# Kernel tuning notes

Measured on AMD Instinct MI355X. Metric: run time of the kernel, lower is better.

The kernel has to match this reference:

```python
import jax, jax.numpy as jnp
import numpy as np

B, TGT, SRC = 16, 1024, 1024
TGT_DIM, SRC_DIM = 1024, 1024


def setup_inputs() -> dict:
    key = jax.random.key(0)
    k1, k2, k3, k4 = jax.random.split(key, 4)
    source = jax.random.normal(k1, (B, TGT, TGT_DIM), dtype=jnp.float32)
    memory_bank = jax.random.normal(k2, (B, SRC, SRC_DIM), dtype=jnp.float32)
    # lengths in [1, SRC] so every row has at least one valid position
    memory_lengths = jax.random.randint(k3, (B,), 1, SRC + 1)
    # nn.Linear(tgt_enc_dim, src_enc_dim, bias=False): weight [src_dim, tgt_dim]
    W_in = jax.random.normal(k4, (SRC_DIM, TGT_DIM), dtype=jnp.float32) / np.sqrt(TGT_DIM)
    return {"source": source, "memory_bank": memory_bank,
            "memory_lengths": memory_lengths, "W_in": W_in}


def reference(source, memory_bank, memory_lengths, W_in):
    # general attention: score = (h_t W_in^T) @ h_s^T
    h_t = jnp.einsum('btd,ed->bte', source, W_in)          # [B, TGT, SRC_DIM]
    align = jnp.einsum('bte,bse->bts', h_t, memory_bank)   # [B, TGT, SRC]
    # sequence mask: valid where j < length
    valid = jnp.arange(SRC)[None, :] < memory_lengths[:, None]  # [B, SRC]
    align = jnp.where(valid[:, None, :], align, -jnp.inf)
    return jax.nn.softmax(align, axis=-1)                  # [B, TGT, SRC]
```

## Files before the change

kernel.cpp:

```cpp
#include <hip/hip_runtime.h>
#include <hip/hip_bf16.h>

typedef __bf16 bf16;
typedef __bf16 bf16x8 __attribute__((ext_vector_type(8)));
typedef __bf16 bf16x4 __attribute__((ext_vector_type(4)));
typedef float  f32x4  __attribute__((ext_vector_type(4)));
typedef float  f32x16 __attribute__((ext_vector_type(16)));

struct hl { bf16 h, l; };
__device__ __forceinline__ hl split1(float v) {
    hl r;
    r.h = (bf16)v;
    r.l = (bf16)(v - (float)r.h);
    return r;
}

__device__ __forceinline__ void glds16(const void* g, void* l) {
    __builtin_amdgcn_global_load_lds(
        (const __attribute__((address_space(1))) void*)g,
        (__attribute__((address_space(3))) void*)l, 16, 0, 0);
}

template<int AMODE, int BMODE, int OMODE>
__global__ __launch_bounds__(256, 4) void gemm3(
    const float* __restrict__ Af, const bf16* __restrict__ Agh, const bf16* __restrict__ Agl,
    const float* __restrict__ Bf, const bf16* __restrict__ Bgh, const bf16* __restrict__ Bgl,
    float* __restrict__ Cf, bf16* __restrict__ Cgh, bf16* __restrict__ Cgl,
    int M, int N, int K, long sAz, long sBz, long sCz, int nbm, int nbn)
{
    constexpr int LDA = AMODE ? 32 : 40;
    constexpr int LDB = BMODE ? 32 : 40;
    __shared__ __align__(16) bf16 Ah[128 * LDA];
    __shared__ __align__(16) bf16 Al[128 * LDA];
    __shared__ __align__(16) bf16 Bh[128 * LDB];
    __shared__ __align__(16) bf16 Bl[128 * LDB];

    const int tid  = threadIdx.x;
    const int lane = tid & 63;
    const int wid  = tid >> 6;
    const int wm   = wid >> 1;
    const int wn   = wid & 1;

    const int qq = gridDim.x >> 3;
    const int sw = (blockIdx.x & 7) * qq + (blockIdx.x >> 3);
    const int z  = sw / (nbm * nbn);
    const int tt = sw % (nbm * nbn);
    const int m0 = (tt / nbn) * 128;
    const int n0 = (tt % nbn) * 128;

    const int r0  = tid >> 2;
    const int c0s = ((((tid & 3) * 16) ^ ((r0 & 6) << 3)) >> 1);

    const float* aF[4]; const float* bF[4];
    const bf16 *aH0, *aH1, *aL0, *aL1, *bH0, *bH1, *bL0, *bL1;
    if constexpr (AMODE == 0) {
#pragma unroll
        for (int j = 0; j < 4; ++j) {
            const int idx = j * 256 + tid;
            aF[j] = Af + (long)z * sAz + (long)(m0 + (idx >> 3)) * K + (idx & 7) * 4;
        }
    } else {
        aH0 = Agh + (long)z * sAz + (long)(m0 + r0) * K + c0s;
        aH1 = aH0 + (long)64 * K;
        aL0 = Agl + (long)z * sAz + (long)(m0 + r0) * K + c0s;
        aL1 = aL0 + (long)64 * K;
    }
    if constexpr (BMODE == 0) {
#pragma unroll
        for (int j = 0; j < 4; ++j) {
            const int idx = j * 256 + tid;
            bF[j] = Bf + (long)z * sBz + (long)(n0 + (idx >> 3)) * K + (idx & 7) * 4;
        }
    } else {
        bH0 = Bgh + (long)z * sBz + (long)(n0 + r0) * K + c0s;
        bH1 = bH0 + (long)64 * K;
        bL0 = Bgl + (long)z * sBz + (long)(n0 + r0) * K + c0s;
        bL1 = bL0 + (long)64 * K;
    }

    const int lr32 = lane & 31;
    const int kb8  = (lane >> 5) * 8;
    const int swA  = AMODE ? ((lr32 & 6) << 2) : 0;
    const int swB  = BMODE ? ((lr32 & 6) << 2) : 0;
    const int aRow0 = (wm * 64 + lr32) * LDA;
    const int aRow1 = aRow0 + 32 * LDA;
    const int bRow0 = (wn * 64 + lr32) * LDB;
    const int bRow1 = bRow0 + 32 * LDB;

    f32x16 acc[2][2];
#pragma unroll
    for (int i = 0; i < 2; ++i)
#pragma unroll
        for (int j = 0; j < 2; ++j) acc[i][j] = (f32x16)0.0f;

    for (int kt = 0; kt < K; kt += 32) {
        __syncthreads();
        if constexpr (AMODE == 1) {
            glds16(aH0, &Ah[tid * 8]); glds16(aH1, &Ah[(256 + tid) * 8]);
            glds16(aL0, &Al[tid * 8]); glds16(aL1, &Al[(256 + tid) * 8]);
            aH0 += 32; aH1 += 32; aL0 += 32; aL1 += 32;
        } else {
#pragma unroll
            for (int j = 0; j < 4; ++j) {
                const int idx = j * 256 + tid;
                const int r = idx >> 3, c = (idx & 7) * 4;
                const float4 v = *(const float4*)aF[j]; aF[j] += 32;
                bf16x4 h, l;
                hl s0 = split1(v.x); h.x = s0.h; l.x = s0.l;
                hl s1 = split1(v.y); h.y = s1.h; l.y = s1.l;
                hl s2 = split1(v.z); h.z = s2.h; l.z = s2.l;
                hl s3 = split1(v.w); h.w = s3.h; l.w = s3.l;
                *(bf16x4*)&Ah[r * LDA + c] = h;
                *(bf16x4*)&Al[r * LDA + c] = l;
            }
        }
        if constexpr (BMODE == 1) {
            glds16(bH0, &Bh[tid * 8]); glds16(bH1, &Bh[(256 + tid) * 8]);
            glds16(bL0, &Bl[tid * 8]); glds16(bL1, &Bl[(256 + tid) * 8]);
            bH0 += 32; bH1 += 32; bL0 += 32; bL1 += 32;
        } else {
#pragma unroll
            for (int j = 0; j < 4; ++j) {
                const int idx = j * 256 + tid;
                const int r = idx >> 3, c = (idx & 7) * 4;
                const float4 v = *(const float4*)bF[j]; bF[j] += 32;
                bf16x4 h, l;
                hl s0 = split1(v.x); h.x = s0.h; l.x = s0.l;
                hl s1 = split1(v.y); h.y = s1.h; l.y = s1.l;
                hl s2 = split1(v.z); h.z = s2.h; l.z = s2.l;
                hl s3 = split1(v.w); h.w = s3.h; l.w = s3.l;
                *(bf16x4*)&Bh[r * LDB + c] = h;
                *(bf16x4*)&Bl[r * LDB + c] = l;
            }
        }
        __syncthreads();

#pragma unroll
        for (int kk = 0; kk < 2; ++kk) {
            const int ca = (kk * 16 + kb8) ^ swA;
            const int cb = (kk * 16 + kb8) ^ swB;
            bf16x8 ah0 = *(const bf16x8*)&Ah[aRow0 + ca];
            bf16x8 ah1 = *(const bf16x8*)&Ah[aRow1 + ca];
            bf16x8 al0 = *(const bf16x8*)&Al[aRow0 + ca];
            bf16x8 al1 = *(const bf16x8*)&Al[aRow1 + ca];
            bf16x8 bh0 = *(const bf16x8*)&Bh[bRow0 + cb];
            bf16x8 bh1 = *(const bf16x8*)&Bh[bRow1 + cb];
            bf16x8 bl0 = *(const bf16x8*)&Bl[bRow0 + cb];
            bf16x8 bl1 = *(const bf16x8*)&Bl[bRow1 + cb];

            acc[0][0] = __builtin_amdgcn_mfma_f32_32x32x16_bf16(ah0, bh0, acc[0][0], 0, 0, 0);
            acc[0][1] = __builtin_amdgcn_mfma_f32_32x32x16_bf16(ah0, bh1, acc[0][1], 0, 0, 0);
            acc[1][0] = __builtin_amdgcn_mfma_f32_32x32x16_bf16(ah1, bh0, acc[1][0], 0, 0, 0);
            acc[1][1] = __builtin_amdgcn_mfma_f32_32x32x16_bf16(ah1, bh1, acc[1][1], 0, 0, 0);

            acc[0][0] = __builtin_amdgcn_mfma_f32_32x32x16_bf16(al0, bh0, acc[0][0], 0, 0, 0);
            acc[0][1] = __builtin_amdgcn_mfma_f32_32x32x16_bf16(al0, bh1, acc[0][1], 0, 0, 0);
            acc[1][0] = __builtin_amdgcn_mfma_f32_32x32x16_bf16(al1, bh0, acc[1][0], 0, 0, 0);
            acc[1][1] = __builtin_amdgcn_mfma_f32_32x32x16_bf16(al1, bh1, acc[1][1], 0, 0, 0);

            acc[0][0] = __builtin_amdgcn_mfma_f32_32x32x16_bf16(ah0, bl0, acc[0][0], 0, 0, 0);
            acc[0][1] = __builtin_amdgcn_mfma_f32_32x32x16_bf16(ah0, bl1, acc[0][1], 0, 0, 0);
            acc[1][0] = __builtin_amdgcn_mfma_f32_32x32x16_bf16(ah1, bl0, acc[1][0], 0, 0, 0);
            acc[1][1] = __builtin_amdgcn_mfma_f32_32x32x16_bf16(ah1, bl1, acc[1][1], 0, 0, 0);
        }
    }

    const int drow = 4 * (lane >> 5);
#pragma unroll
    for (int i = 0; i < 2; ++i)
#pragma unroll
        for (int j = 0; j < 2; ++j) {
            f32x16 a = acc[i][j];
#pragma unroll
            for (int q = 0; q < 16; ++q) {
                const int row = m0 + wm * 64 + i * 32 + (q & 3) + 8 * (q >> 2) + drow;
                const int col = n0 + wn * 64 + j * 32 + lr32;
                const long off = (long)z * sCz + (long)row * N + col;
                if constexpr (OMODE == 0) {
                    Cf[off] = a[q];
                } else {
                    hl s = split1(a[q]);
                    Cgh[off] = s.h; Cgl[off] = s.l;
                }
            }
        }
}

__global__ __launch_bounds__(256) void split_pair(
    const float* __restrict__ x, bf16* __restrict__ h, bf16* __restrict__ l, long n4)
{
    long i = (long)blockIdx.x * 256 + threadIdx.x;
    const long stride = (long)gridDim.x * 256;
    for (; i < n4; i += stride) {
        const float4 v = ((const float4*)x)[i];
        bf16x4 hh, ll;
        hl s0 = split1(v.x); hh.x = s0.h; ll.x = s0.l;
        hl s1 = split1(v.y); hh.y = s1.h; ll.y = s1.l;
        hl s2 = split1(v.z); hh.z = s2.h; ll.z = s2.l;
        hl s3 = split1(v.w); hh.w = s3.h; ll.w = s3.l;
        ((bf16x4*)h)[i] = hh;
        ((bf16x4*)l)[i] = ll;
    }
}

__global__ __launch_bounds__(256) void softmax_wave(
    float* __restrict__ data, const int* __restrict__ lens)
{
    const int tid  = threadIdx.x;
    const int lane = tid & 63;
    const int row  = blockIdx.x * 4 + (tid >> 6);
    const int len  = lens[row >> 10];
    float* p = data + (long)row * 1024;

    float4 v[4];
#pragma unroll
    for (int q = 0; q < 4; ++q) v[q] = *(const float4*)(p + 4 * (lane + 64 * q));

    float m = -INFINITY;
#pragma unroll
    for (int q = 0; q < 4; ++q) {
        const int base = 4 * (lane + 64 * q);
        if (base + 0 < len) m = fmaxf(m, v[q].x);
        if (base + 1 < len) m = fmaxf(m, v[q].y);
        if (base + 2 < len) m = fmaxf(m, v[q].z);
        if (base + 3 < len) m = fmaxf(m, v[q].w);
    }
#pragma unroll
    for (int off = 32; off >= 1; off >>= 1) m = fmaxf(m, __shfl_xor(m, off));

    float s = 0.0f;
    float4 e[4];
#pragma unroll
    for (int q = 0; q < 4; ++q) {
        const int base = 4 * (lane + 64 * q);
        e[q].x = (base + 0 < len) ? __expf(v[q].x - m) : 0.0f;
        e[q].y = (base + 1 < len) ? __expf(v[q].y - m) : 0.0f;
        e[q].z = (base + 2 < len) ? __expf(v[q].z - m) : 0.0f;
        e[q].w = (base + 3 < len) ? __expf(v[q].w - m) : 0.0f;
        s += e[q].x + e[q].y + e[q].z + e[q].w;
    }
#pragma unroll
    for (int off = 32; off >= 1; off >>= 1) s += __shfl_xor(s, off);

    const float inv = 1.0f / s;
#pragma unroll
    for (int q = 0; q < 4; ++q) {
        float4 o; o.x = e[q].x * inv; o.y = e[q].y * inv; o.z = e[q].z * inv; o.w = e[q].w * inv;
        *(float4*)(p + 4 * (lane + 64 * q)) = o;
    }
}

__global__ __launch_bounds__(256) void gemm_bt_split(
    const float* __restrict__ A, const float* __restrict__ Bmat,
    float* __restrict__ C, int M, int N, int K,
    long sAz, long sBz, long sCz)
{
    __shared__ __align__(16) bf16 Ah[128][40];
    __shared__ __align__(16) bf16 Al[128][40];
    __shared__ __align__(16) bf16 Bh[128][40];
    __shared__ __align__(16) bf16 Bl[128][40];

    const int tid  = threadIdx.x;
    const int lane = tid & 63;
    const int wid  = tid >> 6;
    const int wm   = wid >> 1;
    const int wn   = wid & 1;
    const int z    = blockIdx.z;
    const long aBase = (long)z * sAz;
    const long bBase = (long)z * sBz;
    const long cBase = (long)z * sCz;
    const int m0 = blockIdx.x * 128;
    const int n0 = blockIdx.y * 128;

    f32x4 acc[4][4];
#pragma unroll
    for (int i = 0; i < 4; ++i)
#pragma unroll
        for (int j = 0; j < 4; ++j) acc[i][j] = (f32x4)0.0f;

    const int lr = lane & 15;
    const int lk = (lane >> 4) * 8;

    for (int kt = 0; kt < K; kt += 32) {
        __syncthreads();
#pragma unroll
        for (int j = 0; j < 4; ++j) {
            const int idx = j * 256 + tid;
            const int r   = idx >> 3;
            const int c   = (idx & 7) * 4;
            const float4 va = *(const float4*)(A    + aBase + (long)(m0 + r) * K + kt + c);
            const float4 vb = *(const float4*)(Bmat + bBase + (long)(n0 + r) * K + kt + c);
            bf16x4 ah, al, bh, bl;
            hl a0 = split1(va.x); ah.x = a0.h; al.x = a0.l;
            hl a1 = split1(va.y); ah.y = a1.h; al.y = a1.l;
            hl a2 = split1(va.z); ah.z = a2.h; al.z = a2.l;
            hl a3 = split1(va.w); ah.w = a3.h; al.w = a3.l;
            hl b0 = split1(vb.x); bh.x = b0.h; bl.x = b0.l;
            hl b1 = split1(vb.y); bh.y = b1.h; bl.y = b1.l;
            hl b2 = split1(vb.z); bh.z = b2.h; bl.z = b2.l;
            hl b3 = split1(vb.w); bh.w = b3.h; bl.w = b3.l;
            *(bf16x4*)&Ah[r][c] = ah; *(bf16x4*)&Al[r][c] = al;
            *(bf16x4*)&Bh[r][c] = bh; *(bf16x4*)&Bl[r][c] = bl;
        }
        __syncthreads();

        bf16x8 afh[4], afl[4], bfh[4], bfl[4];
#pragma unroll
        for (int i = 0; i < 4; ++i) {
            afh[i] = *(const bf16x8*)&Ah[wm * 64 + i * 16 + lr][lk];
            afl[i] = *(const bf16x8*)&Al[wm * 64 + i * 16 + lr][lk];
            bfh[i] = *(const bf16x8*)&Bh[wn * 64 + i * 16 + lr][lk];
            bfl[i] = *(const bf16x8*)&Bl[wn * 64 + i * 16 + lr][lk];
        }
#pragma unroll
        for (int i = 0; i < 4; ++i)
#pragma unroll
            for (int j = 0; j < 4; ++j) {
                acc[i][j] = __builtin_amdgcn_mfma_f32_16x16x32_bf16(afh[i], bfh[j], acc[i][j], 0, 0, 0);
                acc[i][j] = __builtin_amdgcn_mfma_f32_16x16x32_bf16(afl[i], bfh[j], acc[i][j], 0, 0, 0);
                acc[i][j] = __builtin_amdgcn_mfma_f32_16x16x32_bf16(afh[i], bfl[j], acc[i][j], 0, 0, 0);
            }
    }

    const int rr = (lane >> 4) * 4;
#pragma unroll
    for (int i = 0; i < 4; ++i)
#pragma unroll
        for (int j = 0; j < 4; ++j)
#pragma unroll
            for (int q = 0; q < 4; ++q)
                C[cBase + (long)(m0 + wm * 64 + i * 16 + rr + q) * N
                        + (n0 + wn * 64 + j * 16 + (lane & 15))] = acc[i][j][q];
}

extern "C" void kernel_launch(void* const* d_in, const int* in_sizes, int n_in,
                              void* d_out, int out_size, void* d_ws, size_t ws_size,
                              hipStream_t stream)
{
    const float* source         = (const float*)d_in[0];
    const float* memory_bank    = (const float*)d_in[1];
    const int*   memory_lengths = (const int*)  d_in[2];
    const float* W_in           = (const float*)d_in[3];
    float* out = (float*)d_out;
    char*  ws  = (char*)d_ws;

    const size_t MB = 1ull << 20;
    const long Z = 1024 * 1024;

    if (ws_size >= 197 * MB) {
        bf16* htH = (bf16*)(ws);            bf16* htL = (bf16*)(ws + 32 * MB);
        bf16* WH  = (bf16*)(ws + 64 * MB);  bf16* WL  = (bf16*)(ws + 66 * MB);
        bf16* mbH = (bf16*)(ws + 68 * MB);  bf16* mbL = (bf16*)(ws + 100 * MB);
        bf16* srH = (bf16*)(ws + 132 * MB); bf16* srL = (bf16*)(ws + 164 * MB);
        split_pair<<<512,  256, 0, stream>>>(W_in,        WH,  WL,  (1l  << 20) / 4);
        split_pair<<<2048, 256, 0, stream>>>(memory_bank, mbH, mbL, (16l << 20) / 4);
        split_pair<<<2048, 256, 0, stream>>>(source,      srH, srL, (16l << 20) / 4);
        gemm3<1,1,1><<<1024, 256, 0, stream>>>(nullptr, srH, srL, nullptr, WH, WL,
            nullptr, htH, htL, 16384, 1024, 1024, 0, 0, 0, 128, 8);
        gemm3<1,1,0><<<1024, 256, 0, stream>>>(nullptr, htH, htL, nullptr, mbH, mbL,
            out, nullptr, nullptr, 1024, 1024, 1024, Z, Z, Z, 8, 8);
    } else if (ws_size >= 133 * MB) {
        bf16* htH = (bf16*)(ws);            bf16* htL = (bf16*)(ws + 32 * MB);
        bf16* WH  = (bf16*)(ws + 64 * MB);  bf16* WL  = (bf16*)(ws + 66 * MB);
        bf16* mbH = (bf16*)(ws + 68 * MB);  bf16* mbL = (bf16*)(ws + 100 * MB);
        split_pair<<<512,  256, 0, stream>>>(W_in,        WH,  WL,  (1l  << 20) / 4);
        split_pair<<<2048, 256, 0, stream>>>(memory_bank, mbH, mbL, (16l << 20) / 4);
        gemm3<0,1,1><<<1024, 256, 0, stream>>>(source, nullptr, nullptr, nullptr, WH, WL,
            nullptr, htH, htL, 16384, 1024, 1024, 0, 0, 0, 128, 8);
        gemm3<1,1,0><<<1024, 256, 0, stream>>>(nullptr, htH, htL, nullptr, mbH, mbL,
            out, nullptr, nullptr, 1024, 1024, 1024, Z, Z, Z, 8, 8);
    } else if (ws_size >= 69 * MB) {
        bf16* htH = (bf16*)(ws);            bf16* htL = (bf16*)(ws + 32 * MB);
        bf16* WH  = (bf16*)(ws + 64 * MB);  bf16* WL  = (bf16*)(ws + 66 * MB);
        split_pair<<<512, 256, 0, stream>>>(W_in, WH, WL, (1l << 20) / 4);
        gemm3<0,1,1><<<1024, 256, 0, stream>>>(source, nullptr, nullptr, nullptr, WH, WL,
            nullptr, htH, htL, 16384, 1024, 1024, 0, 0, 0, 128, 8);
        gemm3<1,0,0><<<1024, 256, 0, stream>>>(nullptr, htH, htL, memory_bank, nullptr, nullptr,
            out, nullptr, nullptr, 1024, 1024, 1024, Z, Z, Z, 8, 8);
    } else {
        float* ht = (float*)ws;
        gemm_bt_split<<<dim3(128, 8, 1), 256, 0, stream>>>(
            source, W_in, ht, 16384, 1024, 1024, 0, 0, 0);
        gemm_bt_split<<<dim3(8, 8, 16), 256, 0, stream>>>(
            ht, memory_bank, out, 1024, 1024, 1024, Z, Z, Z);
    }

    softmax_wave<<<4096, 256, 0, stream>>>(out, memory_lengths);
}
```

Baseline: 413.5 us.

## Double-buffer LDS tiles in split-bf16 GEMM and fuse the three split kernels

The GEMM now keeps two LDS stages per operand. The next k-tile is prefetched into the alternate buffer while MFMAs consume the current one, and only one barrier is issued per iteration instead of two. The aim is to overlap global-to-LDS loads with compute. The three fp32-to-bf16 hi/lo split launches are also merged into a single kernel to cut launch overhead and tail effects. The cost is twice the LDS per block, which may reduce occupancy against the 4-blocks launch bound. There is also a question of whether the async global_load_lds writes are properly waited on before the next iteration reads the buffer.

New measurement: 415.2 us. No clear change (+0.4%).

```diff
diff --git a/kernel.cpp b/kernel.cpp
--- a/kernel.cpp
+++ b/kernel.cpp
@@ -30,10 +30,10 @@
 {
     constexpr int LDA = AMODE ? 32 : 40;
     constexpr int LDB = BMODE ? 32 : 40;
-    __shared__ __align__(16) bf16 Ah[128 * LDA];
-    __shared__ __align__(16) bf16 Al[128 * LDA];
-    __shared__ __align__(16) bf16 Bh[128 * LDB];
-    __shared__ __align__(16) bf16 Bl[128 * LDB];
+    __shared__ __align__(16) bf16 Ah[2][128 * LDA];
+    __shared__ __align__(16) bf16 Al[2][128 * LDA];
+    __shared__ __align__(16) bf16 Bh[2][128 * LDB];
+    __shared__ __align__(16) bf16 Bl[2][128 * LDB];
 
     const int tid  = threadIdx.x;
     const int lane = tid & 63;
@@ -78,26 +78,10 @@
         bL1 = bL0 + (long)64 * K;
     }
 
-    const int lr32 = lane & 31;
-    const int kb8  = (lane >> 5) * 8;
-    const int swA  = AMODE ? ((lr32 & 6) << 2) : 0;
-    const int swB  = BMODE ? ((lr32 & 6) << 2) : 0;
-    const int aRow0 = (wm * 64 + lr32) * LDA;
-    const int aRow1 = aRow0 + 32 * LDA;
-    const int bRow0 = (wn * 64 + lr32) * LDB;
-    const int bRow1 = bRow0 + 32 * LDB;
-
-    f32x16 acc[2][2];
-#pragma unroll
-    for (int i = 0; i < 2; ++i)
-#pragma unroll
-        for (int j = 0; j < 2; ++j) acc[i][j] = (f32x16)0.0f;
-
-    for (int kt = 0; kt < K; kt += 32) {
-        __syncthreads();
+    auto stageA = [&](int s) {
         if constexpr (AMODE == 1) {
-            glds16(aH0, &Ah[tid * 8]); glds16(aH1, &Ah[(256 + tid) * 8]);
-            glds16(aL0, &Al[tid * 8]); glds16(aL1, &Al[(256 + tid) * 8]);
+            glds16(aH0, &Ah[s][tid * 8]); glds16(aH1, &Ah[s][(256 + tid) * 8]);
+            glds16(aL0, &Al[s][tid * 8]); glds16(aL1, &Al[s][(256 + tid) * 8]);
             aH0 += 32; aH1 += 32; aL0 += 32; aL1 += 32;
         } else {
 #pragma unroll
@@ -110,13 +94,15 @@
                 hl s1 = split1(v.y); h.y = s1.h; l.y = s1.l;
                 hl s2 = split1(v.z); h.z = s2.h; l.z = s2.l;
                 hl s3 = split1(v.w); h.w = s3.h; l.w = s3.l;
-                *(bf16x4*)&Ah[r * LDA + c] = h;
-                *(bf16x4*)&Al[r * LDA + c] = l;
+                *(bf16x4*)&Ah[s][r * LDA + c] = h;
+                *(bf16x4*)&Al[s][r * LDA + c] = l;
             }
         }
+    };
+    auto stageB = [&](int s) {
         if constexpr (BMODE == 1) {
-            glds16(bH0, &Bh[tid * 8]); glds16(bH1, &Bh[(256 + tid) * 8]);
-            glds16(bL0, &Bl[tid * 8]); glds16(bL1, &Bl[(256 + tid) * 8]);
+            glds16(bH0, &Bh[s][tid * 8]); glds16(bH1, &Bh[s][(256 + tid) * 8]);
+            glds16(bL0, &Bl[s][tid * 8]); glds16(bL1, &Bl[s][(256 + tid) * 8]);
             bH0 += 32; bH1 += 32; bL0 += 32; bL1 += 32;
         } else {
 #pragma unroll
@@ -129,24 +115,48 @@
                 hl s1 = split1(v.y); h.y = s1.h; l.y = s1.l;
                 hl s2 = split1(v.z); h.z = s2.h; l.z = s2.l;
                 hl s3 = split1(v.w); h.w = s3.h; l.w = s3.l;
-                *(bf16x4*)&Bh[r * LDB + c] = h;
-                *(bf16x4*)&Bl[r * LDB + c] = l;
+                *(bf16x4*)&Bh[s][r * LDB + c] = h;
+                *(bf16x4*)&Bl[s][r * LDB + c] = l;
             }
         }
-        __syncthreads();
-
+    };
+
+    const int lr32 = lane & 31;
+    const int kb8  = (lane >> 5) * 8;
+    const int swA  = AMODE ? ((lr32 & 6) << 2) : 0;
+    const int swB  = BMODE ? ((lr32 & 6) << 2) : 0;
+    const int aRow0 = (wm * 64 + lr32) * LDA;
+    const int aRow1 = aRow0 + 32 * LDA;
+    const int bRow0 = (wn * 64 + lr32) * LDB;
+    const int bRow1 = bRow0 + 32 * LDB;
+
+    f32x16 acc[2][2];
+#pragma unroll
+    for (int i = 0; i < 2; ++i)
+#pragma unroll
+        for (int j = 0; j < 2; ++j) acc[i][j] = (f32x16)0.0f;
+
+    stageA(0); stageB(0);
+    __syncthreads();
+
+    int cur = 0;
+    for (int kt = 0; kt < K; kt += 32) {
+        if (kt + 32 < K) { stageA(cur ^ 1); stageB(cur ^ 1); }
+
+        const bf16* AhC = Ah[cur]; const bf16* AlC = Al[cur];
+        const bf16* BhC = Bh[cur]; const bf16* BlC = Bl[cur];
 #pragma unroll
         for (int kk = 0; kk < 2; ++kk) {
             const int ca = (kk * 16 + kb8) ^ swA;
             const int cb = (kk * 16 + kb8) ^ swB;
-            bf16x8 ah0 = *(const bf16x8*)&Ah[aRow0 + ca];
-            bf16x8 ah1 = *(const bf16x8*)&Ah[aRow1 + ca];
-            bf16x8 al0 = *(const bf16x8*)&Al[aRow0 + ca];
-            bf16x8 al1 = *(const bf16x8*)&Al[aRow1 + ca];
-            bf16x8 bh0 = *(const bf16x8*)&Bh[bRow0 + cb];
-            bf16x8 bh1 = *(const bf16x8*)&Bh[bRow1 + cb];
-            bf16x8 bl0 = *(const bf16x8*)&Bl[bRow0 + cb];
-            bf16x8 bl1 = *(const bf16x8*)&Bl[bRow1 + cb];
+            bf16x8 ah0 = *(const bf16x8*)&AhC[aRow0 + ca];
+            bf16x8 ah1 = *(const bf16x8*)&AhC[aRow1 + ca];
+            bf16x8 al0 = *(const bf16x8*)&AlC[aRow0 + ca];
+            bf16x8 al1 = *(const bf16x8*)&AlC[aRow1 + ca];
+            bf16x8 bh0 = *(const bf16x8*)&BhC[bRow0 + cb];
+            bf16x8 bh1 = *(const bf16x8*)&BhC[bRow1 + cb];
+            bf16x8 bl0 = *(const bf16x8*)&BlC[bRow0 + cb];
+            bf16x8 bl1 = *(const bf16x8*)&BlC[bRow1 + cb];
 
             acc[0][0] = __builtin_amdgcn_mfma_f32_32x32x16_bf16(ah0, bh0, acc[0][0], 0, 0, 0);
             acc[0][1] = __builtin_amdgcn_mfma_f32_32x32x16_bf16(ah0, bh1, acc[0][1], 0, 0, 0);
@@ -163,6 +173,8 @@
             acc[1][0] = __builtin_amdgcn_mfma_f32_32x32x16_bf16(ah1, bl0, acc[1][0], 0, 0, 0);
             acc[1][1] = __builtin_amdgcn_mfma_f32_32x32x16_bf16(ah1, bl1, acc[1][1], 0, 0, 0);
         }
+        __syncthreads();
+        cur ^= 1;
     }
 
     const int drow = 4 * (lane >> 5);
@@ -184,6 +196,32 @@
                 }
             }
         }
+}
+
+__global__ __launch_bounds__(256) void split3(
+    const float* __restrict__ w,   bf16* __restrict__ wh,  bf16* __restrict__ wl,
+    const float* __restrict__ mb,  bf16* __restrict__ mbh, bf16* __restrict__ mbl,
+    const float* __restrict__ src, bf16* __restrict__ sh,  bf16* __restrict__ sl)
+{
+    const long NW = 262144;
+    const long NB = 4194304;
+    const long NT = NW + 2 * NB;
+    long i = (long)blockIdx.x * 256 + threadIdx.x;
+    const long stride = (long)gridDim.x * 256;
+    for (; i < NT; i += stride) {
+        const float* x; bf16* h; bf16* l; long j;
+        if (i < NW)            { x = w;   h = wh;  l = wl;  j = i; }
+        else if (i < NW + NB)  { x = mb;  h = mbh; l = mbl; j = i - NW; }
+        else                   { x = src; h = sh;  l = sl;  j = i - NW - NB; }
+        const float4 v = ((const float4*)x)[j];
+        bf16x4 hh, ll;
+        hl s0 = split1(v.x); hh.x = s0.h; ll.x = s0.l;
+        hl s1 = split1(v.y); hh.y = s1.h; ll.y = s1.l;
+        hl s2 = split1(v.z); hh.z = s2.h; ll.z = s2.l;
+        hl s3 = split1(v.w); hh.w = s3.h; ll.w = s3.l;
+        ((bf16x4*)h)[j] = hh;
+        ((bf16x4*)l)[j] = ll;
+    }
 }
 
 __global__ __launch_bounds__(256) void split_pair(
@@ -352,9 +390,8 @@
         bf16* WH  = (bf16*)(ws + 64 * MB);  bf16* WL  = (bf16*)(ws + 66 * MB);
         bf16* mbH = (bf16*)(ws + 68 * MB);  bf16* mbL = (bf16*)(ws + 100 * MB);
         bf16* srH = (bf16*)(ws + 132 * MB); bf16* srL = (bf16*)(ws + 164 * MB);
-        split_pair<<<512,  256, 0, stream>>>(W_in,        WH,  WL,  (1l  << 20) / 4);
-        split_pair<<<2048, 256, 0, stream>>>(memory_bank, mbH, mbL, (16l << 20) / 4);
-        split_pair<<<2048, 256, 0, stream>>>(source,      srH, srL, (16l << 20) / 4);
+        split3<<<2048, 256, 0, stream>>>(W_in, WH, WL, memory_bank, mbH, mbL,
+                                         source, srH, srL);
         gemm3<1,1,1><<<1024, 256, 0, stream>>>(nullptr, srH, srL, nullptr, WH, WL,
             nullptr, htH, htL, 16384, 1024, 1024, 0, 0, 0, 128, 8);
         gemm3<1,1,0><<<1024, 256, 0, stream>>>(nullptr, htH, htL, nullptr, mbH, mbL,
```
